# Kernel tuning notes

Measured on AMD Instinct MI355X. Metric: run time of the kernel, lower is better.

The kernel has to match this reference:

```python
import jax, jax.numpy as jnp
import numpy as np

DIM = 1024
GROUPS = 32
EPS = 1e-5


def setup_inputs() -> dict:
    key = jax.random.key(0)
    ks = jax.random.split(key, 12)
    b, c, h, w = 16, DIM, 32, 32  # h*w must equal DIM for GroupNorm(32, dim) on (b, hw, c)
    x = jax.random.normal(ks[0], (b, c, h, w), dtype=jnp.float32)
    # GroupNorm affine params: num_channels = dim (applied along hw axis, which == dim)
    gamma = jnp.ones((DIM,), dtype=jnp.float32)
    beta = jnp.zeros((DIM,), dtype=jnp.float32)
    init = lambda k: jax.random.normal(k, (DIM, DIM), dtype=jnp.float32) * 0.02
    Wq, Wk, Wv, Wo = init(ks[1]), init(ks[2]), init(ks[3]), init(ks[4])
    bq = jax.random.normal(ks[5], (DIM,), dtype=jnp.float32) * 0.02
    bk = jax.random.normal(ks[6], (DIM,), dtype=jnp.float32) * 0.02
    bv = jax.random.normal(ks[7], (DIM,), dtype=jnp.float32) * 0.02
    bo = jax.random.normal(ks[8], (DIM,), dtype=jnp.float32) * 0.02
    return {"x": x, "gamma": gamma, "beta": beta,
            "Wq": Wq, "bq": bq, "Wk": Wk, "bk": bk,
            "Wv": Wv, "bv": bv, "Wo": Wo, "bo": bo}


def _group_norm(x, gamma, beta):
    # x: (b, N, c) where N == num_channels (torch GroupNorm normalizes groups along dim 1)
    b, N, c = x.shape
    xg = x.reshape(b, GROUPS, (N // GROUPS) * c)
    mean = xg.mean(-1, keepdims=True)
    var = xg.var(-1, keepdims=True)
    xn = ((xg - mean) * jax.lax.rsqrt(var + EPS)).reshape(b, N, c)
    return xn * gamma[None, :, None] + beta[None, :, None]


def reference(x, gamma, beta, Wq, bq, Wk, bk, Wv, bv, Wo, bo):
    b, c, h, w = x.shape
    xs = x.reshape(b, c, h * w).transpose(0, 2, 1)  # (b, N, c), N = h*w
    norm_x = _group_norm(xs, gamma, beta)
    q = norm_x @ Wq.T + bq
    k = norm_x @ Wk.T + bk
    v = norm_x @ Wv.T + bv
    attn = jnp.einsum('bqd,bkd->bqk', q, k) * (c ** -0.5)
    attn = jax.nn.softmax(attn, axis=-1)
    # Faithful to original: 'bqk,bvd->bqd' sums k and v independently (no contraction between them)
    out = jnp.einsum('bqk,bvd->bqd', attn, v)
    out = out @ Wo.T + bo  # Dropout(p=0.0) is identity
    return out.transpose(0, 2, 1).reshape(b, c, h, w)
```

## Files before the change

### kernel.cpp

```cpp
#include <hip/hip_runtime.h>


#define BATCH 16
#define CH    1024
#define NHW   1024
#define G     32
#define NPG   32
#define EPG   (NPG*CH)
#define EPSV  1e-5f
#define GRID  (BATCH*G)
#define TPB   1024

__device__ __forceinline__ void coh_store_f32(float* p, float v) {
    __hip_atomic_store((unsigned*)p, __float_as_uint(v), __ATOMIC_RELAXED, __HIP_MEMORY_SCOPE_AGENT);
}
__device__ __forceinline__ void coh_load_f32x2(const float* p, float* d0, float* d1) {
    unsigned long long u = __hip_atomic_load((const unsigned long long*)p,
                                             __ATOMIC_RELAXED, __HIP_MEMORY_SCOPE_AGENT);
    *d0 = __uint_as_float((unsigned)(u & 0xffffffffu));
    *d1 = __uint_as_float((unsigned)(u >> 32));
}

__device__ __forceinline__ void batch_barrier(int* ctr, int expected)
{
    __syncthreads();
    if (threadIdx.x == 0) {
        __hip_atomic_fetch_add(ctr, 1, __ATOMIC_RELAXED, __HIP_MEMORY_SCOPE_AGENT);
        while (__hip_atomic_load(ctr, __ATOMIC_RELAXED, __HIP_MEMORY_SCOPE_AGENT) < expected)
            __builtin_amdgcn_s_sleep(1);
    }
    __syncthreads();
}

__global__ __launch_bounds__(TPB, 8) void fused_all(
    const float* __restrict__ x, const float* __restrict__ gamma,
    const float* __restrict__ beta,
    const float* __restrict__ Wv, const float* __restrict__ bv,
    const float* __restrict__ Wo, const float* __restrict__ bo,
    float* __restrict__ colsum, float* __restrict__ S,
    float* __restrict__ out, int* __restrict__ bar0, int* __restrict__ bar1)
{
    const int blk  = blockIdx.x;
    const int t    = threadIdx.x;
    const int lane = t & 63, wave = t >> 6;
    const int b    = blk >> 5;

    __shared__ float smem[CH];
    __shared__ float r1[16], r2[16], rb[16];

    {
        const int g  = blk & 31;
        const int n4 = t & 7;
        const int c0 = t >> 3;

        const float4* xg = reinterpret_cast<const float4*>(x + (size_t)b * (CH * NHW) + g * NPG);
        const float4  gm = reinterpret_cast<const float4*>(gamma + g * NPG)[n4];

        float4 vb[8];
        #pragma unroll
        for (int k = 0; k < 8; k++)
            vb[k] = xg[(c0 + k * 128) * (NHW / 4) + n4];

        float s1 = 0.f, s2 = 0.f;
        #pragma unroll
        for (int k = 0; k < 8; k++) {
            const float4 v = vb[k];
            const int ch = c0 + k * 128;
            s1 += v.x + v.y + v.z + v.w;
            s2 += v.x * v.x + v.y * v.y + v.z * v.z + v.w * v.w;
            float p = v.x * gm.x + v.y * gm.y + v.z * gm.z + v.w * gm.w;
            p += __shfl_xor(p, 1);
            p += __shfl_xor(p, 2);
            p += __shfl_xor(p, 4);
            if (n4 == 0) smem[ch] = p;
        }
        float bsum = beta[t];
        #pragma unroll
        for (int m = 1; m < 64; m <<= 1) {
            s1 += __shfl_xor(s1, m); s2 += __shfl_xor(s2, m); bsum += __shfl_xor(bsum, m);
        }
        if (lane == 0) { r1[wave] = s1; r2[wave] = s2; rb[wave] = bsum; }
        __syncthreads();

        float S1 = 0.f, S2 = 0.f, SB = 0.f;
        #pragma unroll
        for (int w = 0; w < 16; w++) { S1 += r1[w]; S2 += r2[w]; SB += rb[w]; }
        const float mean = S1 * (1.f / EPG);
        const float var  = S2 * (1.f / EPG) - mean * mean;
        const float inv  = rsqrtf(var + EPSV);
        float sg = gm.x + gm.y + gm.z + gm.w;
        sg += __shfl_xor(sg, 1);
        sg += __shfl_xor(sg, 2);
        sg += __shfl_xor(sg, 4);
        const float cshare = SB * (1.f / 32.f) - inv * mean * sg;

        atomicAdd(&colsum[b * CH + t], inv * smem[t] + cshare);
    }
    batch_barrier(&bar0[b * 32], G);

    {
        const int rg = blk & 31;
        if (t < 512) {
            float a0, a1;
            coh_load_f32x2(colsum + b * CH + t * 2, &a0, &a1);
            smem[t * 2 + 0] = a0; smem[t * 2 + 1] = a1;
        }
        __syncthreads();

        const int d0 = rg * 32 + wave * 2;
        const float4* cs4 = reinterpret_cast<const float4*>(smem);
        #pragma unroll
        for (int j = 0; j < 2; j++) {
            const int d = d0 + j;
            const float4* wrow = reinterpret_cast<const float4*>(Wv + (size_t)d * CH);
            float a = 0.f;
            #pragma unroll
            for (int i = 0; i < 4; i++) {
                int e4 = i * 64 + lane;
                float4 w = wrow[e4];
                float4 c = cs4[e4];
                a += w.x * c.x + w.y * c.y + w.z * c.z + w.w * c.w;
            }
            #pragma unroll
            for (int m = 1; m < 64; m <<= 1) a += __shfl_xor(a, m);
            if (lane == 0)
                coh_store_f32(&S[b * CH + d], a + (float)NHW * bv[d]);
        }
    }
    batch_barrier(&bar1[b * 32], G);

    {
        const int rg = blk & 31;
        if (t < 512) {
            float a0, a1;
            coh_load_f32x2(S + b * CH + t * 2, &a0, &a1);
            smem[t * 2 + 0] = a0; smem[t * 2 + 1] = a1;
        }
        __syncthreads();

        const int d0 = rg * 32 + wave * 2;
        const float4* s4 = reinterpret_cast<const float4*>(smem);
        #pragma unroll
        for (int j = 0; j < 2; j++) {
            const int d = d0 + j;
            const float4* wrow = reinterpret_cast<const float4*>(Wo + (size_t)d * CH);
            float a = 0.f;
            #pragma unroll
            for (int i = 0; i < 4; i++) {
                int e4 = i * 64 + lane;
                float4 w = wrow[e4];
                float4 c = s4[e4];
                a += w.x * c.x + w.y * c.y + w.z * c.z + w.w * c.w;
            }
            #pragma unroll
            for (int m = 1; m < 64; m <<= 1) a += __shfl_xor(a, m);
            const float val = a + bo[d];
            float4 v4 = make_float4(val, val, val, val);
            float4* op = reinterpret_cast<float4*>(out + ((size_t)b * CH + d) * NHW);
            #pragma unroll
            for (int i = 0; i < 4; i++) op[i * 64 + lane] = v4;
        }
    }
}

extern "C" void kernel_launch(void* const* d_in, const int* in_sizes, int n_in,
                              void* d_out, int out_size, void* d_ws, size_t ws_size,
                              hipStream_t stream)
{
    const float* x     = (const float*)d_in[0];
    const float* gamma = (const float*)d_in[1];
    const float* beta  = (const float*)d_in[2];
    const float* Wv    = (const float*)d_in[7];
    const float* bv    = (const float*)d_in[8];
    const float* Wo    = (const float*)d_in[9];
    const float* bo    = (const float*)d_in[10];
    float* out = (float*)d_out;

    char* ws = (char*)d_ws;
    float* colsum = (float*)ws;
    int*   bar0   = (int*)(ws + 65536);
    int*   bar1   = (int*)(ws + 65536 + 2048);
    float* Sbuf   = (float*)(ws + 65536 + 4096);

    hipMemsetAsync(ws, 0, 65536 + 4096, stream);
    fused_all<<<GRID, TPB, 0, stream>>>(x, gamma, beta, Wv, bv, Wo, bo,
                                        colsum, Sbuf, out, bar0, bar1);
}
```

Measured before the change: 160.0 us.

## Read x in contiguous rows per block and split group stats across blocks

After: 164.7 us. 2.9% more time.

```diff
diff --git a/kernel.cpp b/kernel.cpp
--- a/kernel.cpp
+++ b/kernel.cpp
@@ -11,6 +11,10 @@
 #define GRID  (BATCH*G)
 #define TPB   1024
 
+__device__ __forceinline__ float coh_load_f32(const float* p) {
+    unsigned u = __hip_atomic_load((const unsigned*)p, __ATOMIC_RELAXED, __HIP_MEMORY_SCOPE_AGENT);
+    return __uint_as_float(u);
+}
 __device__ __forceinline__ void coh_store_f32(float* p, float v) {
     __hip_atomic_store((unsigned*)p, __float_as_uint(v), __ATOMIC_RELAXED, __HIP_MEMORY_SCOPE_AGENT);
 }
@@ -38,68 +42,116 @@
     const float* __restrict__ Wv, const float* __restrict__ bv,
     const float* __restrict__ Wo, const float* __restrict__ bo,
     float* __restrict__ colsum, float* __restrict__ S,
-    float* __restrict__ out, int* __restrict__ bar0, int* __restrict__ bar1)
+    float* __restrict__ out,
+    float* __restrict__ gs1, float* __restrict__ gs2,
+    int* __restrict__ bar0, int* __restrict__ bar1, int* __restrict__ bar2)
 {
     const int blk  = blockIdx.x;
     const int t    = threadIdx.x;
     const int lane = t & 63, wave = t >> 6;
     const int b    = blk >> 5;
-
+    const int slab = blk & 31;
+
+    __shared__ float pg [32][33];
+    __shared__ float q1s[32][33];
+    __shared__ float q2s[32][33];
+    __shared__ float sgam[32], invs[32], rb[16];
+    __shared__ float Ksh;
     __shared__ float smem[CH];
-    __shared__ float r1[16], r2[16], rb[16];
-
-    {
-        const int g  = blk & 31;
-        const int n4 = t & 7;
-        const int c0 = t >> 3;
-
-        const float4* xg = reinterpret_cast<const float4*>(x + (size_t)b * (CH * NHW) + g * NPG);
-        const float4  gm = reinterpret_cast<const float4*>(gamma + g * NPG)[n4];
-
-        float4 vb[8];
-        #pragma unroll
-        for (int k = 0; k < 8; k++)
-            vb[k] = xg[(c0 + k * 128) * (NHW / 4) + n4];
-
-        float s1 = 0.f, s2 = 0.f;
-        #pragma unroll
-        for (int k = 0; k < 8; k++) {
-            const float4 v = vb[k];
-            const int ch = c0 + k * 128;
-            s1 += v.x + v.y + v.z + v.w;
-            s2 += v.x * v.x + v.y * v.y + v.z * v.z + v.w * v.w;
-            float p = v.x * gm.x + v.y * gm.y + v.z * gm.z + v.w * gm.w;
-            p += __shfl_xor(p, 1);
-            p += __shfl_xor(p, 2);
-            p += __shfl_xor(p, 4);
-            if (n4 == 0) smem[ch] = p;
-        }
+
+    {
+        const int chA = slab * 32 + wave * 2;
+        const float4* rowA = reinterpret_cast<const float4*>(x + ((size_t)b * CH + chA) * NHW);
+        const float4* rowB = rowA + (NHW / 4);
+        const float4* gamma4 = reinterpret_cast<const float4*>(gamma);
+
+        float4 a4[4], c4[4], g4[4];
+        #pragma unroll
+        for (int i = 0; i < 4; i++) a4[i] = rowA[lane + i * 64];
+        #pragma unroll
+        for (int i = 0; i < 4; i++) c4[i] = rowB[lane + i * 64];
+        #pragma unroll
+        for (int i = 0; i < 4; i++) g4[i] = gamma4[lane + i * 64];
+
         float bsum = beta[t];
         #pragma unroll
-        for (int m = 1; m < 64; m <<= 1) {
-            s1 += __shfl_xor(s1, m); s2 += __shfl_xor(s2, m); bsum += __shfl_xor(bsum, m);
-        }
-        if (lane == 0) { r1[wave] = s1; r2[wave] = s2; rb[wave] = bsum; }
-        __syncthreads();
-
-        float S1 = 0.f, S2 = 0.f, SB = 0.f;
-        #pragma unroll
-        for (int w = 0; w < 16; w++) { S1 += r1[w]; S2 += r2[w]; SB += rb[w]; }
-        const float mean = S1 * (1.f / EPG);
-        const float var  = S2 * (1.f / EPG) - mean * mean;
-        const float inv  = rsqrtf(var + EPSV);
-        float sg = gm.x + gm.y + gm.z + gm.w;
-        sg += __shfl_xor(sg, 1);
-        sg += __shfl_xor(sg, 2);
-        sg += __shfl_xor(sg, 4);
-        const float cshare = SB * (1.f / 32.f) - inv * mean * sg;
-
-        atomicAdd(&colsum[b * CH + t], inv * smem[t] + cshare);
+        for (int m = 1; m < 64; m <<= 1) bsum += __shfl_xor(bsum, m);
+        if (lane == 0) rb[wave] = bsum;
+
+        #pragma unroll
+        for (int i = 0; i < 4; i++) {
+            const int g = i * 8 + (lane >> 3);
+            const float4 v = a4[i], u = c4[i], gm = g4[i];
+            float pA = v.x * gm.x + v.y * gm.y + v.z * gm.z + v.w * gm.w;
+            float sA = v.x + v.y + v.z + v.w;
+            float qA = v.x * v.x + v.y * v.y + v.z * v.z + v.w * v.w;
+            float pB = u.x * gm.x + u.y * gm.y + u.z * gm.z + u.w * gm.w;
+            float sB = u.x + u.y + u.z + u.w;
+            float qB = u.x * u.x + u.y * u.y + u.z * u.z + u.w * u.w;
+            #pragma unroll
+            for (int m = 1; m < 8; m <<= 1) {
+                pA += __shfl_xor(pA, m); sA += __shfl_xor(sA, m); qA += __shfl_xor(qA, m);
+                pB += __shfl_xor(pB, m); sB += __shfl_xor(sB, m); qB += __shfl_xor(qB, m);
+            }
+            if ((lane & 7) == 0) {
+                const int cl = wave * 2;
+                pg [cl][g] = pA; q1s[cl][g] = sA; q2s[cl][g] = qA;
+                pg [cl + 1][g] = pB; q1s[cl + 1][g] = sB; q2s[cl + 1][g] = qB;
+            }
+        }
+        if (t < 256) {
+            float4 gm = gamma4[t];
+            float s = gm.x + gm.y + gm.z + gm.w;
+            s += __shfl_xor(s, 1);
+            s += __shfl_xor(s, 2);
+            s += __shfl_xor(s, 4);
+            if ((t & 7) == 0) sgam[t >> 3] = s;
+        }
+        __syncthreads();
+
+        {
+            const int g  = t >> 5;
+            const int ch = t & 31;
+            float v1 = q1s[ch][g], v2 = q2s[ch][g];
+            #pragma unroll
+            for (int m = 1; m < 32; m <<= 1) { v1 += __shfl_xor(v1, m); v2 += __shfl_xor(v2, m); }
+            if (ch == 0) {
+                atomicAdd(&gs1[b * G + g], v1);
+                atomicAdd(&gs2[b * G + g], v2);
+            }
+        }
     }
     batch_barrier(&bar0[b * 32], G);
 
     {
-        const int rg = blk & 31;
+        if (t < 32) {
+            const float s1 = coh_load_f32(&gs1[b * G + t]);
+            const float s2 = coh_load_f32(&gs2[b * G + t]);
+            const float mean = s1 * (1.f / EPG);
+            const float var  = s2 * (1.f / EPG) - mean * mean;
+            const float inv  = rsqrtf(var + EPSV);
+            invs[t] = inv;
+            float term = inv * mean * sgam[t];
+            #pragma unroll
+            for (int m = 1; m < 32; m <<= 1) term += __shfl_xor(term, m);
+            if (t == 0) {
+                float bs = 0.f;
+                #pragma unroll
+                for (int w = 0; w < 16; w++) bs += rb[w];
+                Ksh = bs - term;
+            }
+        }
+        __syncthreads();
+        const int ch = t >> 5, j = t & 31;
+        float v = invs[j] * pg[ch][j];
+        #pragma unroll
+        for (int m = 1; m < 32; m <<= 1) v += __shfl_xor(v, m);
+        if (j == 0)
+            coh_store_f32(&colsum[b * CH + slab * 32 + ch], Ksh + v);
+    }
+    batch_barrier(&bar1[b * 32], G);
+
+    {
         if (t < 512) {
             float a0, a1;
             coh_load_f32x2(colsum + b * CH + t * 2, &a0, &a1);
@@ -107,7 +159,7 @@
         }
         __syncthreads();
 
-        const int d0 = rg * 32 + wave * 2;
+        const int d0 = slab * 32 + wave * 2;
         const float4* cs4 = reinterpret_cast<const float4*>(smem);
         #pragma unroll
         for (int j = 0; j < 2; j++) {
@@ -127,10 +179,9 @@
                 coh_store_f32(&S[b * CH + d], a + (float)NHW * bv[d]);
         }
     }
-    batch_barrier(&bar1[b * 32], G);
-
-    {
-        const int rg = blk & 31;
+    batch_barrier(&bar2[b * 32], G);
+
+    {
         if (t < 512) {
             float a0, a1;
             coh_load_f32x2(S + b * CH + t * 2, &a0, &a1);
@@ -138,7 +189,7 @@
         }
         __syncthreads();
 
-        const int d0 = rg * 32 + wave * 2;
+        const int d0 = slab * 32 + wave * 2;
         const float4* s4 = reinterpret_cast<const float4*>(smem);
         #pragma unroll
         for (int j = 0; j < 2; j++) {
@@ -178,11 +229,15 @@
 
     char* ws = (char*)d_ws;
     float* colsum = (float*)ws;
-    int*   bar0   = (int*)(ws + 65536);
-    int*   bar1   = (int*)(ws + 65536 + 2048);
-    float* Sbuf   = (float*)(ws + 65536 + 4096);
-
-    hipMemsetAsync(ws, 0, 65536 + 4096, stream);
+    float* gs1    = (float*)(ws + 65536);
+    float* gs2    = (float*)(ws + 65536 + 2048);
+    int*   bar0   = (int*)(ws + 65536 + 4096);
+    int*   bar1   = (int*)(ws + 65536 + 6144);
+    int*   bar2   = (int*)(ws + 65536 + 8192);
+    float* Sbuf   = (float*)(ws + 65536 + 10240);
+
+    hipMemsetAsync(ws, 0, 65536 + 10240, stream);
     fused_all<<<GRID, TPB, 0, stream>>>(x, gamma, beta, Wv, bv, Wo, bo,
-                                        colsum, Sbuf, out, bar0, bar1);
-}
+                                        colsum, Sbuf, out, gs1, gs2,
+                                        bar0, bar1, bar2);
+}
```
